# Performance work log

Measured on AMD Instinct MI355X. Metric: run time of the kernel, lower is better.

The kernel has to match this reference:

```python
import jax, jax.numpy as jnp
import numpy as np
from functools import partial

MAX_DEPTH = 100.0
MIN_DEPTH = 0.1
KS = 5  # custom_kernel_size


def _dilate(x, k):
    # max_pool2d(x, k, stride=1, padding=k//2); torch pads with -inf for max pool
    p = k // 2
    return jax.lax.reduce_window(x, -jnp.inf, jax.lax.max,
                                 (1, 1, k, k), (1, 1, 1, 1),
                                 [(0, 0), (0, 0), (p, p), (p, p)])


def _erode(x, k):
    return -_dilate(-x, k)


def _median_blur(x, k):
    # torch impl: conv2d with identity kernels (zero padding) then median over window dim
    p = k // 2
    b, c, h, w = x.shape
    xp = jnp.pad(x, ((0, 0), (0, 0), (p, p), (p, p)))  # zeros, matching conv2d padding
    wins = jnp.stack([xp[:, :, i:i + h, j:j + w]
                      for i in range(k) for j in range(k)], axis=2)  # [b,c,k*k,h,w]
    return jnp.median(wins, axis=2)


def _gaussian_blur5(x):
    # torchvision gaussian_blur(kernel_size=5, sigma=None):
    # sigma = 0.3*((5-1)*0.5 - 1) + 0.8 = 1.1, reflect padding
    sigma = 1.1
    r = jnp.arange(5, dtype=x.dtype) - 2.0
    g1 = jnp.exp(-(r ** 2) / (2.0 * sigma ** 2))
    g1 = g1 / jnp.sum(g1)
    g2 = jnp.outer(g1, g1)  # [5,5]
    xp = jnp.pad(x, ((0, 0), (0, 0), (2, 2), (2, 2)), mode='reflect')
    kern = g2[None, None]  # [O=1, I=1, 5, 5]
    return jax.lax.conv_general_dilated(xp, kern, (1, 1), 'VALID',
                                        dimension_numbers=('NCHW', 'OIHW', 'NCHW'))


def setup_inputs() -> dict:
    key = jax.random.key(0)
    k1, k2 = jax.random.split(key)
    depth = jax.random.uniform(k1, (16, 1, 352, 1216), dtype=jnp.float32) * MAX_DEPTH
    mask = jax.random.uniform(k2, (16, 1, 352, 1216)) < 0.3
    in_depth = jnp.where(mask, depth, 0.0).astype(jnp.float32)
    return {"in_depth": in_depth}


def reference(in_depth):
    # invert
    dm = jnp.where(in_depth > MIN_DEPTH, MAX_DEPTH - in_depth, in_depth)
    # dilation with custom kernel
    dm = _dilate(dm, KS)
    # closing(5) = erode(dilate)
    dm = _erode(_dilate(dm, 5), 5)
    # fill empty pixels with 7x7 dilation
    empty = dm < MIN_DEPTH
    dm = jnp.where(empty, _dilate(dm, 7), dm)
    # median blur 5
    dm = _median_blur(dm, 5)
    # gaussian blur 5 on valid pixels
    blurred = _gaussian_blur5(dm)
    dm = jnp.where(dm > MIN_DEPTH, blurred, dm)
    # invert back
    dm = jnp.where(dm > MIN_DEPTH, MAX_DEPTH - dm, dm)
    return dm
```

## Files before the change

kernel.cpp:

```cpp
#include <hip/hip_runtime.h>
#include <float.h>
#include <math.h>

#define IW 1216
#define IH 352
#define W4 304
#define MIND 0.1f
#define MAXD 100.0f
#define RB 42

__device__ __forceinline__ float4 vmax4(float4 a, float4 b) {
    return make_float4(fmaxf(a.x,b.x), fmaxf(a.y,b.y), fmaxf(a.z,b.z), fmaxf(a.w,b.w));
}
__device__ __forceinline__ float4 vmin4(float4 a, float4 b) {
    return make_float4(fminf(a.x,b.x), fminf(a.y,b.y), fminf(a.z,b.z), fminf(a.w,b.w));
}

#define CE(a,b) { float _l = fminf(a,b), _h = fmaxf(a,b); a = _l; b = _h; }
#define SORT5(a,b,c,d,e) { CE(a,b) CE(d,e) CE(c,e) CE(c,d) CE(a,d) CE(a,c) CE(b,e) CE(b,d) CE(b,c) }
#define MM8(s0,s1,s2,s3,s4,s5,s6,s7) { CE(s0,s1) CE(s2,s3) CE(s4,s5) CE(s6,s7) \
    CE(s0,s2) CE(s0,s4) CE(s0,s6) CE(s1,s7) CE(s3,s7) CE(s5,s7) }
#define MM7(s0,s1,s2,s3,s4,s5,s6) { CE(s0,s1) CE(s2,s3) CE(s4,s5) \
    CE(s0,s2) CE(s0,s4) CE(s0,s6) CE(s1,s6) CE(s3,s6) CE(s5,s6) }

__global__ __launch_bounds__(256, 3) void mega_k(const float4* __restrict__ in,
                                                 float4* __restrict__ out,
                                                 float w0, float w1, float w2) {
    __shared__ float4 A_[RB][41];
    __shared__ float4 B_[RB][39];
    int b  = blockIdx.x;
    int sw = (b & 7) * 440 + (b >> 3);
    int tx = sw % 10; int t2 = sw / 10;
    int ty = t2 % 22; int n  = t2 / 22;
    int x0 = tx * 128, y0 = ty * 16;
    int tid = threadIdx.x;
    const long ib = (long)n * (IH * W4);
    const int xb4 = x0 >> 2;
    const bool interior = (tx >= 1) && (tx <= 8) && (ty >= 1) && (ty <= 20);

    if (interior) {
        for (int i = tid; i < RB * 40; i += 256) {
            int ra = i / 40, ca = i % 40;
            int gy = y0 + ra - 13, gx4 = xb4 + ca - 4;
            float4 v = in[ib + gy * W4 + gx4];
            v.x = v.x > MIND ? MAXD - v.x : v.x;
            v.y = v.y > MIND ? MAXD - v.y : v.y;
            v.z = v.z > MIND ? MAXD - v.z : v.z;
            v.w = v.w > MIND ? MAXD - v.w : v.w;
            A_[ra][ca] = v;
        }
    } else {
        for (int i = tid; i < RB * 40; i += 256) {
            int ra = i / 40, ca = i % 40;
            int gy = y0 + ra - 13, gx4 = xb4 + ca - 4;
            float4 v;
            if ((unsigned)gy < IH && (unsigned)gx4 < W4) {
                v = in[ib + gy * W4 + gx4];
                v.x = v.x > MIND ? MAXD - v.x : v.x;
                v.y = v.y > MIND ? MAXD - v.y : v.y;
                v.z = v.z > MIND ? MAXD - v.z : v.z;
                v.w = v.w > MIND ? MAXD - v.w : v.w;
            } else { v.x = v.y = v.z = v.w = -FLT_MAX; }
            A_[ra][ca] = v;
        }
    }
    __syncthreads();

    for (int i = tid; i < RB * 38; i += 256) {
        int ra = i / 38, cb = i % 38;
        float t[12];
        *(float4*)&t[0] = A_[ra][cb];
        *(float4*)&t[4] = A_[ra][cb + 1];
        *(float4*)&t[8] = A_[ra][cb + 2];
        float core = fmaxf(fmaxf(fmaxf(t[3],t[4]), fmaxf(t[5],t[6])), fmaxf(t[7],t[8]));
        float a12 = fmaxf(t[1], t[2]), a910 = fmaxf(t[9], t[10]);
        float4 o;
        o.x = fmaxf(fmaxf(core, a12), t[0]);
        o.y = fmaxf(fmaxf(core, a12), t[9]);
        o.z = fmaxf(fmaxf(core, t[2]), a910);
        o.w = fmaxf(fmaxf(core, a910), t[11]);
        B_[ra][cb] = o;
    }
    __syncthreads();

    {
        int c = tid % 38, k = tid / 38;
        if (k < 6) {
            int ra0 = 4 + 6 * k;
            float4 w[9];
            #pragma unroll
            for (int j = 0; j < 8; ++j) w[j] = B_[ra0 - 4 + j][c];
            #pragma unroll
            for (int s = 0; s < 6; ++s) {
                if (ra0 + s <= 37) {
                    w[8] = B_[ra0 + 4 + s][c];
                    float4 m = w[0];
                    #pragma unroll
                    for (int j = 1; j < 9; ++j) m = vmax4(m, w[j]);
                    A_[ra0 + s][c + 1] = m;
                    #pragma unroll
                    for (int j = 0; j < 8; ++j) w[j] = w[j + 1];
                }
            }
        }
    }
    __syncthreads();

    for (int i = tid; i < 34 * 36; i += 256) {
        int ra = i / 36 + 4, cb = i % 36;
        float t[12];
        *(float4*)&t[0] = A_[ra][cb + 1];
        *(float4*)&t[4] = A_[ra][cb + 2];
        *(float4*)&t[8] = A_[ra][cb + 3];
        if (!interior) {
            bool rOK = (unsigned)(y0 + ra - 13) < IH;
            #pragma unroll
            for (int kk = 2; kk <= 9; ++kk) {
                int gx = x0 + 4 * cb - 12 + kk;
                t[kk] = (rOK && (unsigned)gx < IW) ? t[kk] : FLT_MAX;
            }
        }
        float m34 = fminf(t[3], t[4]), m56 = fminf(t[5], t[6]), m78 = fminf(t[7], t[8]);
        float4 o;
        o.x = fminf(fminf(t[2], m34), m56);
        o.y = fminf(fminf(m34, m56), t[7]);
        o.z = fminf(fminf(t[4], m56), m78);
        o.w = fminf(fminf(m56, m78), t[9]);
        B_[ra][cb + 1] = o;
    }
    __syncthreads();

    {
        int c = tid % 36, k = tid / 36;
        if (k < 6) {
            int ra0 = 6 + 5 * k;
            float4 w[5];
            #pragma unroll
            for (int j = 0; j < 4; ++j) w[j] = B_[ra0 - 2 + j][c + 1];
            #pragma unroll
            for (int s = 0; s < 5; ++s) {
                w[4] = B_[ra0 + 2 + s][c + 1];
                float4 m = w[0];
                #pragma unroll
                for (int j = 1; j < 5; ++j) m = vmin4(m, w[j]);
                A_[ra0 + s][c + 2] = m;
                #pragma unroll
                for (int j = 0; j < 4; ++j) w[j] = w[j + 1];
            }
        }
    }
    __syncthreads();

    for (int i = tid; i < 30 * 34; i += 256) {
        int ra = i / 34 + 6, cb2 = i % 34;
        float t[12];
        *(float4*)&t[0] = A_[ra][cb2 + 2];
        *(float4*)&t[4] = A_[ra][cb2 + 3];
        *(float4*)&t[8] = A_[ra][cb2 + 4];
        if (!interior) {
            bool rOK = (unsigned)(y0 + ra - 13) < IH;
            #pragma unroll
            for (int kk = 1; kk <= 10; ++kk) {
                int gx = x0 + 4 * cb2 - 8 + kk;
                t[kk] = (rOK && (unsigned)gx < IW) ? t[kk] : -FLT_MAX;
            }
        }
        float core = fmaxf(fmaxf(t[4], t[5]), fmaxf(t[6], t[7]));
        float a23 = fmaxf(t[2], t[3]), a89 = fmaxf(t[8], t[9]);
        float4 o;
        o.x = fmaxf(fmaxf(core, a23), t[1]);
        o.y = fmaxf(fmaxf(core, a23), t[8]);
        o.z = fmaxf(fmaxf(core, t[3]), a89);
        o.w = fmaxf(fmaxf(core, a89), t[10]);
        B_[ra][cb2 + 2] = o;
    }
    __syncthreads();

    {
        int c = tid % 34, k = tid / 34;
        if (k < 6) {
            int ra0 = 9 + 4 * k;
            float4 w[7];
            #pragma unroll
            for (int j = 0; j < 6; ++j) w[j] = B_[ra0 - 3 + j][c + 2];
            #pragma unroll
            for (int s = 0; s < 4; ++s) {
                w[6] = B_[ra0 + 3 + s][c + 2];
                float4 m = w[0];
                #pragma unroll
                for (int j = 1; j < 7; ++j) m = vmax4(m, w[j]);
                float4 cl = A_[ra0 + s][c + 3];
                float4 o;
                o.x = cl.x < MIND ? m.x : cl.x;
                o.y = cl.y < MIND ? m.y : cl.y;
                o.z = cl.z < MIND ? m.z : cl.z;
                o.w = cl.w < MIND ? m.w : cl.w;
                A_[ra0 + s][c + 3] = o;
                #pragma unroll
                for (int j = 0; j < 6; ++j) w[j] = w[j + 1];
            }
        }
    }
    __syncthreads();

    {
        int c = tid % 34, k = tid / 34;
        if (k < 7) {
            int ra0 = 11 + 3 * k;
            int rlen = min(3, 31 - ra0);
            float rows_[5][8];
            auto loadrow = [&](float* rw, int rr) {
                float4 q0 = A_[rr][c + 2], q1 = A_[rr][c + 3], q2 = A_[rr][c + 4];
                float tmp[8] = {q0.z, q0.w, q1.x, q1.y, q1.z, q1.w, q2.x, q2.y};
                if (interior) {
                    #pragma unroll
                    for (int j = 0; j < 8; ++j) rw[j] = tmp[j];
                } else {
                    bool rOK = (unsigned)(y0 + rr - 13) < IH;
                    #pragma unroll
                    for (int j = 0; j < 8; ++j) {
                        int gx = x0 + 4 * c - 6 + j;
                        rw[j] = (rOK && (unsigned)gx < IW) ? tmp[j] : 0.0f;
                    }
                }
            };
            #pragma unroll
            for (int j = 0; j < 4; ++j) loadrow(rows_[j], ra0 - 2 + j);
            #pragma unroll
            for (int st = 0; st < 3; ++st) {
                if (st < rlen) {
                    loadrow(rows_[4], ra0 + 2 + st);
                    float cs[8][5];
                    #pragma unroll
                    for (int j = 0; j < 8; ++j) {
                        float a0 = rows_[0][j], a1 = rows_[1][j], a2 = rows_[2][j],
                              a3 = rows_[3][j], a4 = rows_[4][j];
                        SORT5(a0, a1, a2, a3, a4)
                        cs[j][0] = a0; cs[j][1] = a1; cs[j][2] = a2; cs[j][3] = a3; cs[j][4] = a4;
                    }
                    float rr4[4];
                    #pragma unroll
                    for (int p = 0; p < 4; ++p) {
                        float m[5][5];
                        #pragma unroll
                        for (int i2 = 0; i2 < 5; ++i2) {
                            m[i2][0] = cs[p][i2];     m[i2][1] = cs[p + 1][i2];
                            m[i2][2] = cs[p + 2][i2]; m[i2][3] = cs[p + 3][i2];
                            m[i2][4] = cs[p + 4][i2];
                            SORT5(m[i2][0], m[i2][1], m[i2][2], m[i2][3], m[i2][4])
                        }
                        float s0 = m[0][3], s1 = m[0][4], s2 = m[1][2], s3 = m[1][3];
                        float s4 = m[1][4], s5 = m[2][1], s6 = m[2][2], s7 = m[2][3];
                        MM8(s0, s1, s2, s3, s4, s5, s6, s7)
                        s0 = m[3][0]; s7 = m[3][1];
                        MM8(s0, s1, s2, s3, s4, s5, s6, s7)
                        s0 = m[3][2]; s7 = m[4][0];
                        MM8(s0, s1, s2, s3, s4, s5, s6, s7)
                        s0 = m[4][1];
                        MM7(s0, s1, s2, s3, s4, s5, s6)
                        CE(s1, s2) CE(s3, s4) CE(s1, s3) CE(s2, s4)
                        float mn = fminf(s2, s3), mx = fmaxf(s2, s3);
                        rr4[p] = fmaxf(mn, fminf(mx, s5));
                    }
                    B_[ra0 + st][c + 2] = make_float4(rr4[0], rr4[1], rr4[2], rr4[3]);
                    #pragma unroll
                    for (int j = 0; j < 4; ++j) {
                        #pragma unroll
                        for (int q = 0; q < 8; ++q) rows_[j][q] = rows_[j + 1][q];
                    }
                }
            }
        }
    }
    __syncthreads();

    for (int i = tid; i < 20 * 32; i += 256) {
        int ra = i / 32 + 11, cb3 = i % 32;
        float t[12];
        *(float4*)&t[0] = B_[ra][cb3 + 2];
        *(float4*)&t[4] = B_[ra][cb3 + 3];
        *(float4*)&t[8] = B_[ra][cb3 + 4];
        if (x0 == 0 && cb3 == 0)      { t[2] = t[6]; t[3] = t[5]; }
        if (x0 == 1152 && cb3 == 15)  { t[8] = t[6]; t[9] = t[5]; }
        float4 o;
        o.x = w2 * (t[2] + t[6]) + w1 * (t[3] + t[5]) + w0 * t[4];
        o.y = w2 * (t[3] + t[7]) + w1 * (t[4] + t[6]) + w0 * t[5];
        o.z = w2 * (t[4] + t[8]) + w1 * (t[5] + t[7]) + w0 * t[6];
        o.w = w2 * (t[5] + t[9]) + w1 * (t[6] + t[8]) + w0 * t[7];
        A_[ra][cb3 + 4] = o;
    }
    __syncthreads();

    {
        int c = tid % 32, k = tid / 32;
        int ra0 = 13 + 2 * k;
        #pragma unroll
        for (int s = 0; s < 2; ++s) {
            int ra = ra0 + s;
            int gy = y0 + ra - 13;
            float4 acc = make_float4(0.f, 0.f, 0.f, 0.f);
            #pragma unroll
            for (int d = -2; d <= 2; ++d) {
                int gy2 = gy + d;
                gy2 = gy2 < 0 ? -gy2 : gy2;
                gy2 = gy2 >= IH ? 2 * IH - 2 - gy2 : gy2;
                int ra2 = gy2 - y0 + 13;
                float4 hv = A_[ra2][c + 4];
                float wd = (d == 0) ? w0 : ((d == 1 || d == -1) ? w1 : w2);
                acc.x = fmaf(wd, hv.x, acc.x); acc.y = fmaf(wd, hv.y, acc.y);
                acc.z = fmaf(wd, hv.z, acc.z); acc.w = fmaf(wd, hv.w, acc.w);
            }
            float4 dm = B_[ra][c + 3];
            float4 o;
            { float sv = dm.x > MIND ? acc.x : dm.x; o.x = sv > MIND ? MAXD - sv : sv; }
            { float sv = dm.y > MIND ? acc.y : dm.y; o.y = sv > MIND ? MAXD - sv : sv; }
            { float sv = dm.z > MIND ? acc.z : dm.z; o.z = sv > MIND ? MAXD - sv : sv; }
            { float sv = dm.w > MIND ? acc.w : dm.w; o.w = sv > MIND ? MAXD - sv : sv; }
            int gx4 = xb4 + c;
            if (gx4 < W4) out[ib + (long)gy * W4 + gx4] = o;
        }
    }
}

extern "C" void kernel_launch(void* const* d_in, const int* in_sizes, int n_in,
                              void* d_out, int out_size, void* d_ws, size_t ws_size,
                              hipStream_t stream) {
    const float4* in = (const float4*)d_in[0];
    float4* O = (float4*)d_out;

    float c2 = 2.42f;
    float e1 = expf(-1.0f / c2);
    float e4 = expf(-4.0f / c2);
    float s  = 1.0f + 2.0f * e1 + 2.0f * e4;
    float w0 = 1.0f / s, w1 = e1 / s, w2 = e4 / s;

    mega_k<<<dim3(3520), dim3(256), 0, stream>>>(in, O, w0, w1, w2);
}
```

Baseline: 176.8 us.

## Use a single shared buffer, fuse horizontal passes into loads, and prune median network

The two shared tiles become one, and each stage now holds its results in registers across a barrier before writing back in place. This halves LDS use and the launch bound is raised to four blocks per CU. The first horizontal dilation is fused into the global load, and the horizontal 7-wide dilation and Gaussian passes are computed on the fly inside the vertical passes. The median network is cut down to top/bottom/middle selection of the sorted columns, which needs fewer compare-exchanges. In exchange there are extra barriers, more register pressure under the tighter launch bound, and some horizontal work is recomputed per row.

```diff
diff --git a/kernel.cpp b/kernel.cpp
--- a/kernel.cpp
+++ b/kernel.cpp
@@ -8,6 +8,7 @@
 #define MIND 0.1f
 #define MAXD 100.0f
 #define RB 42
+#define SWD 39
 
 __device__ __forceinline__ float4 vmax4(float4 a, float4 b) {
     return make_float4(fmaxf(a.x,b.x), fmaxf(a.y,b.y), fmaxf(a.z,b.z), fmaxf(a.w,b.w));
@@ -17,17 +18,51 @@
 }
 
 #define CE(a,b) { float _l = fminf(a,b), _h = fmaxf(a,b); a = _l; b = _h; }
+#define FE(a,b) { float _h = fmaxf(a,b), _l = fminf(a,b); a = _h; b = _l; }
 #define SORT5(a,b,c,d,e) { CE(a,b) CE(d,e) CE(c,e) CE(c,d) CE(a,d) CE(a,c) CE(b,e) CE(b,d) CE(b,c) }
 #define MM8(s0,s1,s2,s3,s4,s5,s6,s7) { CE(s0,s1) CE(s2,s3) CE(s4,s5) CE(s6,s7) \
     CE(s0,s2) CE(s0,s4) CE(s0,s6) CE(s1,s7) CE(s3,s7) CE(s5,s7) }
 #define MM7(s0,s1,s2,s3,s4,s5,s6) { CE(s0,s1) CE(s2,s3) CE(s4,s5) \
     CE(s0,s2) CE(s0,s4) CE(s0,s6) CE(s1,s6) CE(s3,s6) CE(s5,s6) }
 
-__global__ __launch_bounds__(256, 3) void mega_k(const float4* __restrict__ in,
+__device__ __forceinline__ void top2_5(float a, float b, float c, float d, float e,
+                                       float& o1, float& o2) {
+    float mab = fmaxf(a,b), nab = fminf(a,b);
+    float mcd = fmaxf(c,d), ncd = fminf(c,d);
+    float hi4 = fmaxf(mab, mcd);
+    float lo2 = fmaxf(fminf(mab, mcd), fmaxf(nab, ncd));
+    o2 = fmaxf(hi4, e);
+    o1 = fmaxf(fminf(hi4, e), lo2);
+}
+__device__ __forceinline__ void bot2_5(float a, float b, float c, float d, float e,
+                                       float& o1, float& o2) {
+    float mab = fmaxf(a,b), nab = fminf(a,b);
+    float mcd = fmaxf(c,d), ncd = fminf(c,d);
+    float lo4 = fminf(nab, ncd);
+    float hi2 = fminf(fmaxf(nab, ncd), fminf(mab, mcd));
+    o2 = fminf(lo4, e);
+    o1 = fminf(fmaxf(lo4, e), hi2);
+}
+__device__ __forceinline__ void top3_5(float a, float b, float c, float d, float e,
+                                       float& o1, float& o2, float& o3) {
+    CE(a,b) CE(c,d) CE(a,c) CE(b,d) CE(a,e) CE(b,c) CE(b,e)
+    o1 = c; o2 = d; o3 = e;
+}
+__device__ __forceinline__ void bot3_5(float a, float b, float c, float d, float e,
+                                       float& o1, float& o2, float& o3) {
+    FE(a,b) FE(c,d) FE(a,c) FE(b,d) FE(a,e) FE(b,c) FE(b,e)
+    o1 = c; o2 = d; o3 = e;
+}
+__device__ __forceinline__ void mid3_5(float a, float b, float c, float d, float e,
+                                       float& o1, float& o2, float& o3) {
+    CE(a,b) CE(c,d) CE(a,c) CE(b,d) CE(a,e) CE(d,e)
+    o1 = b; o2 = c; o3 = d;
+}
+
+__global__ __launch_bounds__(256, 4) void mega_k(const float4* __restrict__ in,
                                                  float4* __restrict__ out,
                                                  float w0, float w1, float w2) {
-    __shared__ float4 A_[RB][41];
-    __shared__ float4 B_[RB][39];
+    __shared__ float4 S[RB][SWD];
     int b  = blockIdx.x;
     int sw = (b & 7) * 440 + (b >> 3);
     int tx = sw % 10; int t2 = sw / 10;
@@ -38,286 +73,323 @@
     const int xb4 = x0 >> 2;
     const bool interior = (tx >= 1) && (tx <= 8) && (ty >= 1) && (ty <= 20);
 
-    if (interior) {
-        for (int i = tid; i < RB * 40; i += 256) {
-            int ra = i / 40, ca = i % 40;
-            int gy = y0 + ra - 13, gx4 = xb4 + ca - 4;
-            float4 v = in[ib + gy * W4 + gx4];
-            v.x = v.x > MIND ? MAXD - v.x : v.x;
-            v.y = v.y > MIND ? MAXD - v.y : v.y;
-            v.z = v.z > MIND ? MAXD - v.z : v.z;
-            v.w = v.w > MIND ? MAXD - v.w : v.w;
-            A_[ra][ca] = v;
-        }
-    } else {
-        for (int i = tid; i < RB * 40; i += 256) {
-            int ra = i / 40, ca = i % 40;
-            int gy = y0 + ra - 13, gx4 = xb4 + ca - 4;
-            float4 v;
-            if ((unsigned)gy < IH && (unsigned)gx4 < W4) {
-                v = in[ib + gy * W4 + gx4];
-                v.x = v.x > MIND ? MAXD - v.x : v.x;
-                v.y = v.y > MIND ? MAXD - v.y : v.y;
-                v.z = v.z > MIND ? MAXD - v.z : v.z;
-                v.w = v.w > MIND ? MAXD - v.w : v.w;
-            } else { v.x = v.y = v.z = v.w = -FLT_MAX; }
-            A_[ra][ca] = v;
+    {
+        int j = tid % 6, r = tid / 6;
+        if (r < RB) {
+            int c0 = 7 * j;
+            int nc = (j == 5) ? 3 : 7;
+            int gy = y0 + r - 13;
+            bool rok = (unsigned)gy < IH;
+            float4 lf[9];
+            #pragma unroll
+            for (int q = 0; q < 9; ++q) {
+                if (q < nc + 2) {
+                    int g = xb4 + c0 - 4 + q;
+                    float4 v;
+                    if (rok && (unsigned)g < W4) {
+                        v = in[ib + gy * W4 + g];
+                        v.x = v.x > MIND ? MAXD - v.x : v.x;
+                        v.y = v.y > MIND ? MAXD - v.y : v.y;
+                        v.z = v.z > MIND ? MAXD - v.z : v.z;
+                        v.w = v.w > MIND ? MAXD - v.w : v.w;
+                    } else { v.x = v.y = v.z = v.w = -FLT_MAX; }
+                    lf[q] = v;
+                }
+            }
+            #pragma unroll
+            for (int s = 0; s < 7; ++s) {
+                if (s < nc) {
+                    float t[12];
+                    *(float4*)&t[0] = lf[s];
+                    *(float4*)&t[4] = lf[s + 1];
+                    *(float4*)&t[8] = lf[s + 2];
+                    float core = fmaxf(fmaxf(fmaxf(t[3],t[4]), fmaxf(t[5],t[6])), fmaxf(t[7],t[8]));
+                    float a12 = fmaxf(t[1], t[2]), a910 = fmaxf(t[9], t[10]);
+                    float4 o;
+                    o.x = fmaxf(fmaxf(core, a12), t[0]);
+                    o.y = fmaxf(fmaxf(core, a12), t[9]);
+                    o.z = fmaxf(fmaxf(core, t[2]), a910);
+                    o.w = fmaxf(fmaxf(core, a910), t[11]);
+                    S[r][c0 + s] = o;
+                }
+            }
         }
     }
     __syncthreads();
 
-    for (int i = tid; i < RB * 38; i += 256) {
-        int ra = i / 38, cb = i % 38;
-        float t[12];
-        *(float4*)&t[0] = A_[ra][cb];
-        *(float4*)&t[4] = A_[ra][cb + 1];
-        *(float4*)&t[8] = A_[ra][cb + 2];
-        float core = fmaxf(fmaxf(fmaxf(t[3],t[4]), fmaxf(t[5],t[6])), fmaxf(t[7],t[8]));
-        float a12 = fmaxf(t[1], t[2]), a910 = fmaxf(t[9], t[10]);
-        float4 o;
-        o.x = fmaxf(fmaxf(core, a12), t[0]);
-        o.y = fmaxf(fmaxf(core, a12), t[9]);
-        o.z = fmaxf(fmaxf(core, t[2]), a910);
-        o.w = fmaxf(fmaxf(core, a910), t[11]);
-        B_[ra][cb] = o;
-    }
-    __syncthreads();
-
     {
         int c = tid % 38, k = tid / 38;
-        if (k < 6) {
-            int ra0 = 4 + 6 * k;
+        int ra0 = 4 + 6 * k;
+        float4 o[6];
+        if (k < 6) {
             float4 w[9];
             #pragma unroll
-            for (int j = 0; j < 8; ++j) w[j] = B_[ra0 - 4 + j][c];
+            for (int q = 0; q < 8; ++q) w[q] = S[ra0 - 4 + q][c];
             #pragma unroll
             for (int s = 0; s < 6; ++s) {
                 if (ra0 + s <= 37) {
-                    w[8] = B_[ra0 + 4 + s][c];
+                    w[8] = S[ra0 + 4 + s][c];
                     float4 m = w[0];
                     #pragma unroll
-                    for (int j = 1; j < 9; ++j) m = vmax4(m, w[j]);
-                    A_[ra0 + s][c + 1] = m;
-                    #pragma unroll
-                    for (int j = 0; j < 8; ++j) w[j] = w[j + 1];
-                }
-            }
-        }
-    }
-    __syncthreads();
-
-    for (int i = tid; i < 34 * 36; i += 256) {
-        int ra = i / 36 + 4, cb = i % 36;
-        float t[12];
-        *(float4*)&t[0] = A_[ra][cb + 1];
-        *(float4*)&t[4] = A_[ra][cb + 2];
-        *(float4*)&t[8] = A_[ra][cb + 3];
-        if (!interior) {
-            bool rOK = (unsigned)(y0 + ra - 13) < IH;
-            #pragma unroll
-            for (int kk = 2; kk <= 9; ++kk) {
-                int gx = x0 + 4 * cb - 12 + kk;
-                t[kk] = (rOK && (unsigned)gx < IW) ? t[kk] : FLT_MAX;
-            }
-        }
-        float m34 = fminf(t[3], t[4]), m56 = fminf(t[5], t[6]), m78 = fminf(t[7], t[8]);
-        float4 o;
-        o.x = fminf(fminf(t[2], m34), m56);
-        o.y = fminf(fminf(m34, m56), t[7]);
-        o.z = fminf(fminf(t[4], m56), m78);
-        o.w = fminf(fminf(m56, m78), t[9]);
-        B_[ra][cb + 1] = o;
-    }
-    __syncthreads();
+                    for (int q = 1; q < 9; ++q) m = vmax4(m, w[q]);
+                    o[s] = m;
+                    #pragma unroll
+                    for (int q = 0; q < 8; ++q) w[q] = w[q + 1];
+                }
+            }
+        }
+        __syncthreads();
+        if (k < 6) {
+            #pragma unroll
+            for (int s = 0; s < 6; ++s)
+                if (ra0 + s <= 37) S[ra0 + s][c] = o[s];
+        }
+        __syncthreads();
+    }
+
+    {
+        float4 o[5];
+        #pragma unroll
+        for (int ii = 0; ii < 5; ++ii) {
+            int i = tid + 256 * ii;
+            if (i < 34 * 36) {
+                int ra = i / 36 + 4, cb = i % 36;
+                float t[12];
+                *(float4*)&t[0] = S[ra][cb];
+                *(float4*)&t[4] = S[ra][cb + 1];
+                *(float4*)&t[8] = S[ra][cb + 2];
+                if (!interior) {
+                    bool rOK = (unsigned)(y0 + ra - 13) < IH;
+                    #pragma unroll
+                    for (int kk = 2; kk <= 9; ++kk) {
+                        int gx = x0 + 4 * cb - 12 + kk;
+                        t[kk] = (rOK && (unsigned)gx < IW) ? t[kk] : FLT_MAX;
+                    }
+                }
+                float m34 = fminf(t[3], t[4]), m56 = fminf(t[5], t[6]), m78 = fminf(t[7], t[8]);
+                float4 oo;
+                oo.x = fminf(fminf(t[2], m34), m56);
+                oo.y = fminf(fminf(m34, m56), t[7]);
+                oo.z = fminf(fminf(t[4], m56), m78);
+                oo.w = fminf(fminf(m56, m78), t[9]);
+                o[ii] = oo;
+            }
+        }
+        __syncthreads();
+        #pragma unroll
+        for (int ii = 0; ii < 5; ++ii) {
+            int i = tid + 256 * ii;
+            if (i < 34 * 36) { int ra = i / 36 + 4, cb = i % 36; S[ra][cb + 1] = o[ii]; }
+        }
+        __syncthreads();
+    }
 
     {
         int c = tid % 36, k = tid / 36;
-        if (k < 6) {
-            int ra0 = 6 + 5 * k;
+        int ra0 = 6 + 5 * k;
+        float4 o[5];
+        if (k < 6) {
             float4 w[5];
             #pragma unroll
-            for (int j = 0; j < 4; ++j) w[j] = B_[ra0 - 2 + j][c + 1];
+            for (int q = 0; q < 4; ++q) w[q] = S[ra0 - 2 + q][c + 1];
             #pragma unroll
             for (int s = 0; s < 5; ++s) {
-                w[4] = B_[ra0 + 2 + s][c + 1];
+                w[4] = S[ra0 + 2 + s][c + 1];
                 float4 m = w[0];
                 #pragma unroll
-                for (int j = 1; j < 5; ++j) m = vmin4(m, w[j]);
-                A_[ra0 + s][c + 2] = m;
+                for (int q = 1; q < 5; ++q) m = vmin4(m, w[q]);
+                o[s] = m;
                 #pragma unroll
-                for (int j = 0; j < 4; ++j) w[j] = w[j + 1];
-            }
-        }
-    }
-    __syncthreads();
-
-    for (int i = tid; i < 30 * 34; i += 256) {
-        int ra = i / 34 + 6, cb2 = i % 34;
-        float t[12];
-        *(float4*)&t[0] = A_[ra][cb2 + 2];
-        *(float4*)&t[4] = A_[ra][cb2 + 3];
-        *(float4*)&t[8] = A_[ra][cb2 + 4];
-        if (!interior) {
-            bool rOK = (unsigned)(y0 + ra - 13) < IH;
-            #pragma unroll
-            for (int kk = 1; kk <= 10; ++kk) {
-                int gx = x0 + 4 * cb2 - 8 + kk;
-                t[kk] = (rOK && (unsigned)gx < IW) ? t[kk] : -FLT_MAX;
-            }
-        }
-        float core = fmaxf(fmaxf(t[4], t[5]), fmaxf(t[6], t[7]));
-        float a23 = fmaxf(t[2], t[3]), a89 = fmaxf(t[8], t[9]);
-        float4 o;
-        o.x = fmaxf(fmaxf(core, a23), t[1]);
-        o.y = fmaxf(fmaxf(core, a23), t[8]);
-        o.z = fmaxf(fmaxf(core, t[3]), a89);
-        o.w = fmaxf(fmaxf(core, a89), t[10]);
-        B_[ra][cb2 + 2] = o;
-    }
-    __syncthreads();
+                for (int q = 0; q < 4; ++q) w[q] = w[q + 1];
+            }
+        }
+        __syncthreads();
+        if (k < 6) {
+            #pragma unroll
+            for (int s = 0; s < 5; ++s) S[ra0 + s][c + 1] = o[s];
+        }
+        __syncthreads();
+    }
 
     {
         int c = tid % 34, k = tid / 34;
-        if (k < 6) {
-            int ra0 = 9 + 4 * k;
-            float4 w[7];
-            #pragma unroll
-            for (int j = 0; j < 6; ++j) w[j] = B_[ra0 - 3 + j][c + 2];
+        int ra0 = 9 + 4 * k;
+        float4 o[4];
+        if (k < 6) {
+            auto hrow = [&](int rr) -> float4 {
+                float t[12];
+                *(float4*)&t[0] = S[rr][c + 1];
+                *(float4*)&t[4] = S[rr][c + 2];
+                *(float4*)&t[8] = S[rr][c + 3];
+                if (!interior) {
+                    bool rOK = (unsigned)(y0 + rr - 13) < IH;
+                    #pragma unroll
+                    for (int kk = 1; kk <= 10; ++kk) {
+                        int gx = x0 + 4 * c - 8 + kk;
+                        t[kk] = (rOK && (unsigned)gx < IW) ? t[kk] : -FLT_MAX;
+                    }
+                }
+                float core = fmaxf(fmaxf(t[4], t[5]), fmaxf(t[6], t[7]));
+                float a23 = fmaxf(t[2], t[3]), a89 = fmaxf(t[8], t[9]);
+                float4 r;
+                r.x = fmaxf(fmaxf(core, a23), t[1]);
+                r.y = fmaxf(fmaxf(core, a23), t[8]);
+                r.z = fmaxf(fmaxf(core, t[3]), a89);
+                r.w = fmaxf(fmaxf(core, a89), t[10]);
+                return r;
+            };
+            float4 hw[7];
+            #pragma unroll
+            for (int q = 0; q < 6; ++q) hw[q] = hrow(ra0 - 3 + q);
             #pragma unroll
             for (int s = 0; s < 4; ++s) {
-                w[6] = B_[ra0 + 3 + s][c + 2];
-                float4 m = w[0];
+                hw[6] = hrow(ra0 + 3 + s);
+                float4 m = hw[0];
                 #pragma unroll
-                for (int j = 1; j < 7; ++j) m = vmax4(m, w[j]);
-                float4 cl = A_[ra0 + s][c + 3];
-                float4 o;
-                o.x = cl.x < MIND ? m.x : cl.x;
-                o.y = cl.y < MIND ? m.y : cl.y;
-                o.z = cl.z < MIND ? m.z : cl.z;
-                o.w = cl.w < MIND ? m.w : cl.w;
-                A_[ra0 + s][c + 3] = o;
+                for (int q = 1; q < 7; ++q) m = vmax4(m, hw[q]);
+                float4 cl = S[ra0 + s][c + 2];
+                float4 oo;
+                oo.x = cl.x < MIND ? m.x : cl.x;
+                oo.y = cl.y < MIND ? m.y : cl.y;
+                oo.z = cl.z < MIND ? m.z : cl.z;
+                oo.w = cl.w < MIND ? m.w : cl.w;
+                o[s] = oo;
                 #pragma unroll
-                for (int j = 0; j < 6; ++j) w[j] = w[j + 1];
-            }
-        }
-    }
-    __syncthreads();
+                for (int q = 0; q < 6; ++q) hw[q] = hw[q + 1];
+            }
+        }
+        __syncthreads();
+        if (k < 6) {
+            #pragma unroll
+            for (int s = 0; s < 4; ++s) S[ra0 + s][c + 2] = o[s];
+        }
+        __syncthreads();
+    }
 
     {
         int c = tid % 34, k = tid / 34;
+        int ra0 = 11 + 3 * k;
+        int rlen = (k == 6) ? 2 : 3;
+        float4 o[3];
         if (k < 7) {
-            int ra0 = 11 + 3 * k;
-            int rlen = min(3, 31 - ra0);
             float rows_[5][8];
             auto loadrow = [&](float* rw, int rr) {
-                float4 q0 = A_[rr][c + 2], q1 = A_[rr][c + 3], q2 = A_[rr][c + 4];
+                float4 q0 = S[rr][c + 1], q1 = S[rr][c + 2], q2 = S[rr][c + 3];
                 float tmp[8] = {q0.z, q0.w, q1.x, q1.y, q1.z, q1.w, q2.x, q2.y};
                 if (interior) {
                     #pragma unroll
-                    for (int j = 0; j < 8; ++j) rw[j] = tmp[j];
+                    for (int j2 = 0; j2 < 8; ++j2) rw[j2] = tmp[j2];
                 } else {
                     bool rOK = (unsigned)(y0 + rr - 13) < IH;
                     #pragma unroll
-                    for (int j = 0; j < 8; ++j) {
-                        int gx = x0 + 4 * c - 6 + j;
-                        rw[j] = (rOK && (unsigned)gx < IW) ? tmp[j] : 0.0f;
+                    for (int j2 = 0; j2 < 8; ++j2) {
+                        int gx = x0 + 4 * c - 6 + j2;
+                        rw[j2] = (rOK && (unsigned)gx < IW) ? tmp[j2] : 0.0f;
                     }
                 }
             };
             #pragma unroll
-            for (int j = 0; j < 4; ++j) loadrow(rows_[j], ra0 - 2 + j);
+            for (int q = 0; q < 4; ++q) loadrow(rows_[q], ra0 - 2 + q);
             #pragma unroll
             for (int st = 0; st < 3; ++st) {
                 if (st < rlen) {
                     loadrow(rows_[4], ra0 + 2 + st);
                     float cs[8][5];
                     #pragma unroll
-                    for (int j = 0; j < 8; ++j) {
-                        float a0 = rows_[0][j], a1 = rows_[1][j], a2 = rows_[2][j],
-                              a3 = rows_[3][j], a4 = rows_[4][j];
+                    for (int j2 = 0; j2 < 8; ++j2) {
+                        float a0 = rows_[0][j2], a1 = rows_[1][j2], a2 = rows_[2][j2],
+                              a3 = rows_[3][j2], a4 = rows_[4][j2];
                         SORT5(a0, a1, a2, a3, a4)
-                        cs[j][0] = a0; cs[j][1] = a1; cs[j][2] = a2; cs[j][3] = a3; cs[j][4] = a4;
+                        cs[j2][0] = a0; cs[j2][1] = a1; cs[j2][2] = a2; cs[j2][3] = a3; cs[j2][4] = a4;
                     }
                     float rr4[4];
                     #pragma unroll
                     for (int p = 0; p < 4; ++p) {
-                        float m[5][5];
-                        #pragma unroll
-                        for (int i2 = 0; i2 < 5; ++i2) {
-                            m[i2][0] = cs[p][i2];     m[i2][1] = cs[p + 1][i2];
-                            m[i2][2] = cs[p + 2][i2]; m[i2][3] = cs[p + 3][i2];
-                            m[i2][4] = cs[p + 4][i2];
-                            SORT5(m[i2][0], m[i2][1], m[i2][2], m[i2][3], m[i2][4])
-                        }
-                        float s0 = m[0][3], s1 = m[0][4], s2 = m[1][2], s3 = m[1][3];
-                        float s4 = m[1][4], s5 = m[2][1], s6 = m[2][2], s7 = m[2][3];
-                        MM8(s0, s1, s2, s3, s4, s5, s6, s7)
-                        s0 = m[3][0]; s7 = m[3][1];
-                        MM8(s0, s1, s2, s3, s4, s5, s6, s7)
-                        s0 = m[3][2]; s7 = m[4][0];
-                        MM8(s0, s1, s2, s3, s4, s5, s6, s7)
-                        s0 = m[4][1];
-                        MM7(s0, s1, s2, s3, s4, s5, s6)
-                        CE(s1, s2) CE(s3, s4) CE(s1, s3) CE(s2, s4)
+                        float s0,s1,s2,s3,s4,s5,s6,s7,g0,g1,g2,g3,g4;
+                        top2_5(cs[p][0],cs[p+1][0],cs[p+2][0],cs[p+3][0],cs[p+4][0], s0, s1);
+                        top3_5(cs[p][1],cs[p+1][1],cs[p+2][1],cs[p+3][1],cs[p+4][1], s2, s3, s4);
+                        mid3_5(cs[p][2],cs[p+1][2],cs[p+2][2],cs[p+3][2],cs[p+4][2], s5, s6, s7);
+                        bot3_5(cs[p][3],cs[p+1][3],cs[p+2][3],cs[p+3][3],cs[p+4][3], g0, g1, g2);
+                        bot2_5(cs[p][4],cs[p+1][4],cs[p+2][4],cs[p+3][4],cs[p+4][4], g3, g4);
+                        MM8(s0,s1,s2,s3,s4,s5,s6,s7)
+                        s0 = g0; s7 = g1;
+                        MM8(s0,s1,s2,s3,s4,s5,s6,s7)
+                        s0 = g2; s7 = g3;
+                        MM8(s0,s1,s2,s3,s4,s5,s6,s7)
+                        s0 = g4;
+                        MM7(s0,s1,s2,s3,s4,s5,s6)
+                        CE(s1,s2) CE(s3,s4) CE(s1,s3) CE(s2,s4)
                         float mn = fminf(s2, s3), mx = fmaxf(s2, s3);
                         rr4[p] = fmaxf(mn, fminf(mx, s5));
                     }
-                    B_[ra0 + st][c + 2] = make_float4(rr4[0], rr4[1], rr4[2], rr4[3]);
-                    #pragma unroll
-                    for (int j = 0; j < 4; ++j) {
+                    o[st] = make_float4(rr4[0], rr4[1], rr4[2], rr4[3]);
+                    #pragma unroll
+                    for (int q = 0; q < 4; ++q) {
                         #pragma unroll
-                        for (int q = 0; q < 8; ++q) rows_[j][q] = rows_[j + 1][q];
-                    }
-                }
-            }
-        }
-    }
-    __syncthreads();
-
-    for (int i = tid; i < 20 * 32; i += 256) {
-        int ra = i / 32 + 11, cb3 = i % 32;
-        float t[12];
-        *(float4*)&t[0] = B_[ra][cb3 + 2];
-        *(float4*)&t[4] = B_[ra][cb3 + 3];
-        *(float4*)&t[8] = B_[ra][cb3 + 4];
-        if (x0 == 0 && cb3 == 0)      { t[2] = t[6]; t[3] = t[5]; }
-        if (x0 == 1152 && cb3 == 15)  { t[8] = t[6]; t[9] = t[5]; }
-        float4 o;
-        o.x = w2 * (t[2] + t[6]) + w1 * (t[3] + t[5]) + w0 * t[4];
-        o.y = w2 * (t[3] + t[7]) + w1 * (t[4] + t[6]) + w0 * t[5];
-        o.z = w2 * (t[4] + t[8]) + w1 * (t[5] + t[7]) + w0 * t[6];
-        o.w = w2 * (t[5] + t[9]) + w1 * (t[6] + t[8]) + w0 * t[7];
-        A_[ra][cb3 + 4] = o;
-    }
-    __syncthreads();
+                        for (int q2 = 0; q2 < 8; ++q2) rows_[q][q2] = rows_[q + 1][q2];
+                    }
+                }
+            }
+        }
+        __syncthreads();
+        if (k < 7) {
+            #pragma unroll
+            for (int st = 0; st < 3; ++st)
+                if (st < rlen) S[ra0 + st][c + 2] = o[st];
+        }
+        __syncthreads();
+    }
 
     {
         int c = tid % 32, k = tid / 32;
         int ra0 = 13 + 2 * k;
+        bool lfix = (tx == 0) && (c == 0);
+        bool rfix = (tx == 9) && (c == 15);
+        auto hgrow = [&](int rr) -> float4 {
+            float4 q0 = S[rr][c + 2], q1 = S[rr][c + 3], q2 = S[rr][c + 4];
+            float t[8] = {q0.z, q0.w, q1.x, q1.y, q1.z, q1.w, q2.x, q2.y};
+            if (lfix) { t[0] = t[4]; t[1] = t[3]; }
+            if (rfix) { t[6] = t[4]; t[7] = t[3]; }
+            float4 r;
+            r.x = w2 * (t[0] + t[4]) + w1 * (t[1] + t[3]) + w0 * t[2];
+            r.y = w2 * (t[1] + t[5]) + w1 * (t[2] + t[4]) + w0 * t[3];
+            r.z = w2 * (t[2] + t[6]) + w1 * (t[3] + t[5]) + w0 * t[4];
+            r.w = w2 * (t[3] + t[7]) + w1 * (t[4] + t[6]) + w0 * t[5];
+            return r;
+        };
+        float4 hw[6];
+        #pragma unroll
+        for (int q = 0; q < 6; ++q) hw[q] = hgrow(ra0 - 2 + q);
+        bool ybt = (ty == 0) || (ty == 21);
+        int gx4 = xb4 + c;
         #pragma unroll
         for (int s = 0; s < 2; ++s) {
             int ra = ra0 + s;
             int gy = y0 + ra - 13;
-            float4 acc = make_float4(0.f, 0.f, 0.f, 0.f);
-            #pragma unroll
-            for (int d = -2; d <= 2; ++d) {
-                int gy2 = gy + d;
-                gy2 = gy2 < 0 ? -gy2 : gy2;
-                gy2 = gy2 >= IH ? 2 * IH - 2 - gy2 : gy2;
-                int ra2 = gy2 - y0 + 13;
-                float4 hv = A_[ra2][c + 4];
-                float wd = (d == 0) ? w0 : ((d == 1 || d == -1) ? w1 : w2);
-                acc.x = fmaf(wd, hv.x, acc.x); acc.y = fmaf(wd, hv.y, acc.y);
-                acc.z = fmaf(wd, hv.z, acc.z); acc.w = fmaf(wd, hv.w, acc.w);
-            }
-            float4 dm = B_[ra][c + 3];
-            float4 o;
-            { float sv = dm.x > MIND ? acc.x : dm.x; o.x = sv > MIND ? MAXD - sv : sv; }
-            { float sv = dm.y > MIND ? acc.y : dm.y; o.y = sv > MIND ? MAXD - sv : sv; }
-            { float sv = dm.z > MIND ? acc.z : dm.z; o.z = sv > MIND ? MAXD - sv : sv; }
-            { float sv = dm.w > MIND ? acc.w : dm.w; o.w = sv > MIND ? MAXD - sv : sv; }
-            int gx4 = xb4 + c;
-            if (gx4 < W4) out[ib + (long)gy * W4 + gx4] = o;
+            float4 bl;
+            if (!ybt) {
+                bl.x = w2 * (hw[s].x + hw[s+4].x) + w1 * (hw[s+1].x + hw[s+3].x) + w0 * hw[s+2].x;
+                bl.y = w2 * (hw[s].y + hw[s+4].y) + w1 * (hw[s+1].y + hw[s+3].y) + w0 * hw[s+2].y;
+                bl.z = w2 * (hw[s].z + hw[s+4].z) + w1 * (hw[s+1].z + hw[s+3].z) + w0 * hw[s+2].z;
+                bl.w = w2 * (hw[s].w + hw[s+4].w) + w1 * (hw[s+1].w + hw[s+3].w) + w0 * hw[s+2].w;
+            } else {
+                float we0 = w2, we1 = w1, we2 = w0, we3 = w1, we4 = w2;
+                if (gy == 0)        { we0 = 0; we1 = 0; we3 = 2*w1; we4 = 2*w2; }
+                else if (gy == 1)   { we0 = 0; we2 = w0 + w2; }
+                else if (gy == 350) { we2 = w0 + w2; we4 = 0; }
+                else if (gy == 351) { we0 = 2*w2; we1 = 2*w1; we3 = 0; we4 = 0; }
+                bl.x = we0*hw[s].x + we1*hw[s+1].x + we2*hw[s+2].x + we3*hw[s+3].x + we4*hw[s+4].x;
+                bl.y = we0*hw[s].y + we1*hw[s+1].y + we2*hw[s+2].y + we3*hw[s+3].y + we4*hw[s+4].y;
+                bl.z = we0*hw[s].z + we1*hw[s+1].z + we2*hw[s+2].z + we3*hw[s+3].z + we4*hw[s+4].z;
+                bl.w = we0*hw[s].w + we1*hw[s+1].w + we2*hw[s+2].w + we3*hw[s+3].w + we4*hw[s+4].w;
+            }
+            float4 dm = S[ra][c + 3];
+            float4 oo;
+            { float sv = dm.x > MIND ? bl.x : dm.x; oo.x = sv > MIND ? MAXD - sv : sv; }
+            { float sv = dm.y > MIND ? bl.y : dm.y; oo.y = sv > MIND ? MAXD - sv : sv; }
+            { float sv = dm.z > MIND ? bl.z : dm.z; oo.z = sv > MIND ? MAXD - sv : sv; }
+            { float sv = dm.w > MIND ? bl.w : dm.w; oo.w = sv > MIND ? MAXD - sv : sv; }
+            if (gx4 < W4) out[ib + (long)gy * W4 + gx4] = oo;
         }
     }
 }
```

New measurement: 172.3 us. -2.6%, faster.
